# Kernel optimization log

Measured on AMD Instinct MI355X. Metric: run time of the kernel, lower is better.

The kernel has to match this reference:

```python
import jax, jax.numpy as jnp
import numpy as np

LEAKY_SLOPE = 0.2  # tf.nn.leaky_relu default alpha
N_NODES = 50000
N_EDGES = 800000
IN_DIM = 128
OUT_DIM = 64
HEADS = 4
MLP_HID = 256
MLP_OUT = 128


def setup_inputs() -> dict:
    key = jax.random.key(0)
    ks = jax.random.split(key, 10)
    node_embeddings = jax.random.normal(ks[0], (N_NODES, IN_DIM), dtype=jnp.float32)
    src = jax.random.randint(ks[1], (N_EDGES,), 0, N_NODES, dtype=jnp.int32)
    dst = jax.random.randint(ks[2], (N_EDGES,), 0, N_NODES, dtype=jnp.int32)
    # glorot-ish scales
    W_n = jax.random.normal(ks[3], (HEADS, IN_DIM, OUT_DIM), dtype=jnp.float32) * (1.0 / np.sqrt(IN_DIM))
    a_src = jax.random.normal(ks[4], (HEADS, OUT_DIM), dtype=jnp.float32) * (1.0 / np.sqrt(OUT_DIM))
    a_dst = jax.random.normal(ks[5], (HEADS, OUT_DIM), dtype=jnp.float32) * (1.0 / np.sqrt(OUT_DIM))
    mlp_W1 = jax.random.normal(ks[6], (HEADS * OUT_DIM, MLP_HID), dtype=jnp.float32) * (1.0 / np.sqrt(HEADS * OUT_DIM))
    mlp_b1 = jnp.zeros((MLP_HID,), dtype=jnp.float32)
    mlp_W2 = jax.random.normal(ks[7], (MLP_HID, MLP_OUT), dtype=jnp.float32) * (1.0 / np.sqrt(MLP_HID))
    mlp_b2 = jnp.zeros((MLP_OUT,), dtype=jnp.float32)
    return {"node_embeddings": node_embeddings, "src": src, "dst": dst,
            "W_n": W_n, "a_src": a_src, "a_dst": a_dst,
            "mlp_W1": mlp_W1, "mlp_b1": mlp_b1, "mlp_W2": mlp_W2, "mlp_b2": mlp_b2}


def _gat_forward(node_embeddings, src, dst, W_n, a_src, a_dst, mlp_W1, mlp_b1, mlp_W2, mlp_b2):
    N = node_embeddings.shape[0]
    # per-head linear transform: [N, H, D]
    h = jnp.einsum('nc,hcd->nhd', node_embeddings, W_n)
    # decomposed attention scores at node level, gathered per edge
    s_src = jnp.einsum('nhd,hd->nh', h, a_src)          # [N, H]
    s_dst = jnp.einsum('nhd,hd->nh', h, a_dst)          # [N, H]
    e = jax.nn.leaky_relu(s_src[src] + s_dst[dst], negative_slope=LEAKY_SLOPE)  # [E, H]
    # segment softmax over incoming edges of each dst node
    e_max = jax.ops.segment_max(e, dst, num_segments=N)          # [N, H], -inf for empty
    ex = jnp.exp(e - e_max[dst])                                  # [E, H]
    den = jax.ops.segment_sum(ex, dst, num_segments=N)            # [N, H]
    m = h[src]                                                    # [E, H, D] messages
    num = jax.ops.segment_sum(ex[:, :, None] * m, dst, num_segments=N)  # [N, H, D]
    safe_den = jnp.where(den > 0, den, 1.0)
    head_out = jax.nn.relu(num / safe_den[:, :, None])            # [N, H, D]
    concat = head_out.reshape(N, -1)                              # [N, H*D]
    hidden = jax.nn.relu(concat @ mlp_W1 + mlp_b1)
    return hidden @ mlp_W2 + mlp_b2                               # [N, MLP_OUT]


def reference(node_embeddings, src, dst, W_n, a_src, a_dst, mlp_W1, mlp_b1, mlp_W2, mlp_b2):
    return _gat_forward(node_embeddings, src, dst, W_n, a_src, a_dst,
                        mlp_W1, mlp_b1, mlp_W2, mlp_b2)
```

## Files before the change

kernel.cpp:

```cpp
#include <hip/hip_runtime.h>

#define LEAKY 0.2f

typedef __attribute__((ext_vector_type(8))) short short8;
typedef __attribute__((ext_vector_type(4))) float floatx4;

__device__ __forceinline__ float bf2f(unsigned short u) {
    return __uint_as_float(((unsigned)u) << 16);
}
__device__ __forceinline__ unsigned short f2bf(float f) {
    unsigned u = __float_as_uint(f);
    unsigned r = (u + 0x7fffu + ((u >> 16) & 1u)) >> 16;
    return (unsigned short)r;
}
__device__ __forceinline__ float relu_nan(float v) { return v < 0.0f ? 0.0f : v; }

__device__ __forceinline__ void gload_lds16(const void* g, void* l) {
    __builtin_amdgcn_global_load_lds((const __attribute__((address_space(1))) void*)g,
                                     (__attribute__((address_space(3))) void*)l, 16, 0, 0);
}

__global__ void k_fill(float* __restrict__ p, float val, int n) {
    int i = blockIdx.x * blockDim.x + threadIdx.x;
    if (i < n) p[i] = val;
}

__global__ void k_zero(int* __restrict__ cnt, int n) {
    int i = blockIdx.x * blockDim.x + threadIdx.x;
    if (i < n) cnt[i] = 0;
}

__global__ void k_cvt_x(const float* __restrict__ X, unsigned short* __restrict__ Xb, int n4) {
    int i = blockIdx.x * blockDim.x + threadIdx.x;
    if (i < n4) {
        float4 v = ((const float4*)X)[i];
        ushort4 o;
        o.x = f2bf(v.x); o.y = f2bf(v.y); o.z = f2bf(v.z); o.w = f2bf(v.w);
        ((ushort4*)Xb)[i] = o;
    }
}

__global__ void k_cvt_wn(const float* __restrict__ Wn, unsigned short* __restrict__ WnT) {
    int col = blockIdx.x, k = threadIdx.x;
    int head = col >> 6, d = col & 63;
    WnT[(size_t)col * 128 + k] = f2bf(Wn[(size_t)head * 8192 + (size_t)k * 64 + d]);
}

__global__ void k_convert(const float* __restrict__ W, unsigned short* __restrict__ WT, int R, int C) {
    int k = threadIdx.x, n = blockIdx.x;
    WT[(size_t)n * R + k] = f2bf(W[(size_t)k * C + n]);
}

__global__ __launch_bounds__(256) void k_scores(
    const unsigned short* __restrict__ h_bf,
    const float* __restrict__ Asrc, const float* __restrict__ Adst,
    float* __restrict__ s_src, float* __restrict__ s_dst, int N) {
    const int lane = threadIdx.x & 63;
    const int wave = threadIdx.x >> 6;
    const int n = blockIdx.x * 4 + wave;
    if (n >= N) return;
    const int head = lane >> 4;
    const int c0 = lane << 2;
    ushort4 hv = *(const ushort4*)(h_bf + (size_t)n * 256 + c0);
    float4 as = *(const float4*)(Asrc + c0);
    float4 ad = *(const float4*)(Adst + c0);
    float h0 = bf2f(hv.x), h1 = bf2f(hv.y), h2 = bf2f(hv.z), h3 = bf2f(hv.w);
    float ps = h0 * as.x + h1 * as.y + h2 * as.z + h3 * as.w;
    float pd = h0 * ad.x + h1 * ad.y + h2 * ad.z + h3 * ad.w;
    for (int m = 1; m < 16; m <<= 1) {
        ps += __shfl_xor(ps, m, 64);
        pd += __shfl_xor(pd, m, 64);
    }
    if ((lane & 15) == 0) {
        s_src[n * 4 + head] = ps;
        s_dst[n * 4 + head] = pd;
    }
}

__global__ void k_hist(const int* __restrict__ dst, int* __restrict__ cnt, int E) {
    int e = blockIdx.x * blockDim.x + threadIdx.x;
    if (e < E) atomicAdd(cnt + dst[e], 1);
}

__global__ __launch_bounds__(256) void k_scan1(
    const int* __restrict__ cnt, int* __restrict__ rowptr, int* __restrict__ bsum, int N) {
    __shared__ int wtot[4];
    const int lane = threadIdx.x & 63, wave = threadIdx.x >> 6;
    const int i = blockIdx.x * 256 + threadIdx.x;
    int v = (i < N) ? cnt[i] : 0;
    int x = v;
    for (int off = 1; off < 64; off <<= 1) {
        int y = __shfl_up(x, off, 64);
        if (lane >= off) x += y;
    }
    if (lane == 63) wtot[wave] = x;
    __syncthreads();
    int wo = 0;
    for (int wv = 0; wv < wave; ++wv) wo += wtot[wv];
    if (i < N) rowptr[i] = wo + x - v;
    if (threadIdx.x == 255) bsum[blockIdx.x] = wo + x;
}
__global__ void k_scan2(int* __restrict__ bsum, int nb) {
    const int lane = threadIdx.x;
    int carry = 0;
    for (int base = 0; base < nb; base += 64) {
        int i = base + lane;
        int v = (i < nb) ? bsum[i] : 0;
        int x = v;
        for (int off = 1; off < 64; off <<= 1) {
            int y = __shfl_up(x, off, 64);
            if (lane >= off) x += y;
        }
        if (i < nb) bsum[i] = carry + x - v;
        carry += __shfl(x, 63, 64);
    }
}
__global__ void k_scan3(int* __restrict__ rowptr, const int* __restrict__ bsum,
                        int* __restrict__ wcnt, int N, int E) {
    int i = blockIdx.x * blockDim.x + threadIdx.x;
    if (i < N) {
        int v = rowptr[i] + bsum[i >> 8];
        rowptr[i] = v;
        wcnt[i] = v;
    }
    if (i == N) rowptr[N] = E;
}

__global__ void k_scatter(const int* __restrict__ src, const int* __restrict__ dst,
                          int* __restrict__ wcnt, int* __restrict__ esrc, int E) {
    int e = blockIdx.x * blockDim.x + threadIdx.x;
    if (e < E) {
        int pos = atomicAdd(wcnt + dst[e], 1);
        esrc[pos] = src[e];
    }
}

__global__ __launch_bounds__(256) void k_agg(
    const float* __restrict__ s_src, const float* __restrict__ s_dst,
    const unsigned short* __restrict__ h_bf,
    const int* __restrict__ rowptr, const int* __restrict__ esrc,
    unsigned short* __restrict__ concat) {
    const int t = threadIdx.x;
    const int lane = t & 63;
    const int wave = t >> 6;
    const int row0 = blockIdx.x * 16;
    const int head = lane >> 4;
    const int c0 = lane << 2;
    const int eslot = lane & 15;
    const int hsel = lane & 48;

    for (int rr = 0; rr < 4; ++rr) {
        const int n = row0 + wave * 4 + rr;
        const int beg = rowptr[n], end = rowptr[n + 1];
        const float sdst = s_dst[n * 4 + head];
        float num0 = 0, num1 = 0, num2 = 0, num3 = 0, den = 0;
        for (int base = beg; base < end; base += 16) {
            const int nn = end - base;
            int sid = 0;
            float my_ex = 0.0f;
            if (eslot < nn) {
                sid = esrc[base + eslot];
                float v = s_src[sid * 4 + head] + sdst;
                v = v > 0.0f ? v : LEAKY * v;
                my_ex = __expf(v);
            }
#pragma unroll
            for (int e = 0; e < 16; ++e) {
                float ex = __shfl(my_ex, hsel | e, 64);
                int s    = __shfl(sid, e, 64);
                ushort4 hv = *(const ushort4*)(h_bf + (size_t)s * 256 + c0);
                num0 += ex * bf2f(hv.x);
                num1 += ex * bf2f(hv.y);
                num2 += ex * bf2f(hv.z);
                num3 += ex * bf2f(hv.w);
                den  += ex;
            }
        }
        const float inv = 1.0f / (den > 0.0f ? den : 1.0f);
        ushort4 o;
        o.x = f2bf(relu_nan(num0 * inv));
        o.y = f2bf(relu_nan(num1 * inv));
        o.z = f2bf(relu_nan(num2 * inv));
        o.w = f2bf(relu_nan(num3 * inv));
        *(ushort4*)(concat + (size_t)n * 256 + c0) = o;
    }
}

template <int K, int MODE>
__global__ __launch_bounds__(256) void k_gemm(
    const unsigned short* __restrict__ A, const unsigned short* __restrict__ BT,
    const float* __restrict__ bias, unsigned short* __restrict__ Cb,
    float* __restrict__ Cf, int N, int ldout) {
    __shared__ unsigned short As[128 * 32];
    __shared__ unsigned short Bs[128 * 32];
    const int t = threadIdx.x;
    const int lane = t & 63;
    const int w = t >> 6;
    const int wy = w >> 1, wx = w & 1;
    const int lm = lane & 15, quad = lane >> 4;
    const int row0 = blockIdx.x * 128;
    const int n0 = blockIdx.y * 128;
    const int srow = lane >> 2;
    const int sk = (lane & 3) * 8;

    floatx4 acc[4][4];
    if (MODE == 0) {
#pragma unroll
        for (int mi = 0; mi < 4; ++mi)
#pragma unroll
            for (int ni = 0; ni < 4; ++ni) acc[mi][ni] = (floatx4){0, 0, 0, 0};
    } else {
#pragma unroll
        for (int ni = 0; ni < 4; ++ni) {
            float b = bias[n0 + wx * 64 + ni * 16 + lm];
#pragma unroll
            for (int mi = 0; mi < 4; ++mi) acc[mi][ni] = (floatx4){b, b, b, b};
        }
    }

    for (int k0 = 0; k0 < K; k0 += 32) {
#pragma unroll
        for (int p = 0; p < 2; ++p) {
            int tr = (p * 4 + w) * 16 + srow;
            int ga = row0 + tr; if (ga >= N) ga = N - 1;
            gload_lds16(A + (size_t)ga * K + k0 + sk,
                        (char*)As + (size_t)tr * 64 + sk * 2);
            gload_lds16(BT + (size_t)(n0 + tr) * K + k0 + sk,
                        (char*)Bs + (size_t)tr * 64 + sk * 2);
        }
        __syncthreads();
        short8 af[4], bfr[4];
#pragma unroll
        for (int mi = 0; mi < 4; ++mi)
            af[mi] = *(const short8*)(As + (size_t)(wy * 64 + mi * 16 + lm) * 32 + quad * 8);
#pragma unroll
        for (int ni = 0; ni < 4; ++ni)
            bfr[ni] = *(const short8*)(Bs + (size_t)(wx * 64 + ni * 16 + lm) * 32 + quad * 8);
#pragma unroll
        for (int mi = 0; mi < 4; ++mi)
#pragma unroll
            for (int ni = 0; ni < 4; ++ni)
                acc[mi][ni] = __builtin_amdgcn_mfma_f32_16x16x32_bf16(af[mi], bfr[ni], acc[mi][ni], 0, 0, 0);
        __syncthreads();
    }

#pragma unroll
    for (int mi = 0; mi < 4; ++mi)
#pragma unroll
        for (int ni = 0; ni < 4; ++ni)
#pragma unroll
            for (int q = 0; q < 4; ++q) {
                int r = row0 + wy * 64 + mi * 16 + quad * 4 + q;
                int c = n0 + wx * 64 + ni * 16 + lm;
                if (r < N) {
                    if (MODE == 0)      Cb[(size_t)r * ldout + c] = f2bf(acc[mi][ni][q]);
                    else if (MODE == 1) Cb[(size_t)r * ldout + c] = f2bf(relu_nan(acc[mi][ni][q]));
                    else                Cf[(size_t)r * ldout + c] = acc[mi][ni][q];
                }
            }
}

extern "C" void kernel_launch(void* const* d_in, const int* in_sizes, int n_in,
                              void* d_out, int out_size, void* d_ws, size_t ws_size,
                              hipStream_t stream) {
    const float* X    = (const float*)d_in[0];
    const int* src    = (const int*)d_in[1];
    const int* dst    = (const int*)d_in[2];
    const float* Wn   = (const float*)d_in[3];
    const float* Asrc = (const float*)d_in[4];
    const float* Adst = (const float*)d_in[5];
    const float* W1   = (const float*)d_in[6];
    const float* b1   = (const float*)d_in[7];
    const float* W2   = (const float*)d_in[8];
    const float* b2   = (const float*)d_in[9];
    float* out = (float*)d_out;

    const int N = in_sizes[0] / 128;
    const int E = in_sizes[1];
    const int NB = (N + 255) / 256;
    const int NR = (N + 127) / 128;

    size_t off = 0;
    char* w = (char*)d_ws;
    unsigned short* h_bf = (unsigned short*)(w + off); off += (size_t)N * 256 * 2;
    float* s_src = (float*)(w + off);                  off += (size_t)N * 4 * 4;
    float* s_dst = (float*)(w + off);                  off += (size_t)N * 4 * 4;
    int* cnt     = (int*)(w + off);                    off += (size_t)N * 4;
    int* rowptr  = (int*)(w + off);                    off += ((size_t)(N + 1) * 4 + 15) & ~15ull;
    int* wcnt    = (int*)(w + off);                    off += (size_t)N * 4;
    int* bsum    = (int*)(w + off);                    off += ((size_t)NB * 4 + 15) & ~15ull;
    int* esrc    = (int*)(w + off);                    off += (size_t)E * 4;
    unsigned short* W1T = (unsigned short*)(w + off);  off += 256 * 256 * 2;
    unsigned short* W2T = (unsigned short*)(w + off);  off += 128 * 256 * 2;
    unsigned short* WnT = (unsigned short*)(w + off);  off += 256 * 128 * 2;
    const size_t required = off;

    if (ws_size < required) {
        k_fill<<<dim3((out_size + 255) / 256), dim3(256), 0, stream>>>(
            out, (float)(ws_size >> 20), out_size);
        return;
    }

    unsigned short* Xb     = (unsigned short*)d_out;
    unsigned short* concat = (unsigned short*)d_out;

    k_zero<<<dim3((N + 255) / 256), dim3(256), 0, stream>>>(cnt, N);
    k_cvt_x<<<dim3((N * 32 + 255) / 256), dim3(256), 0, stream>>>(X, Xb, N * 32);
    k_cvt_wn<<<dim3(256), dim3(128), 0, stream>>>(Wn, WnT);
    k_gemm<128, 0><<<dim3(NR, 2), dim3(256), 0, stream>>>(Xb, WnT, nullptr, h_bf, nullptr, N, 256);
    k_scores<<<dim3((N + 3) / 4), dim3(256), 0, stream>>>(h_bf, Asrc, Adst, s_src, s_dst, N);
    k_hist<<<dim3((E + 255) / 256), dim3(256), 0, stream>>>(dst, cnt, E);
    k_scan1<<<dim3(NB), dim3(256), 0, stream>>>(cnt, rowptr, bsum, N);
    k_scan2<<<dim3(1), dim3(64), 0, stream>>>(bsum, NB);
    k_scan3<<<dim3((N + 256) / 256), dim3(256), 0, stream>>>(rowptr, bsum, wcnt, N, E);
    k_scatter<<<dim3((E + 255) / 256), dim3(256), 0, stream>>>(src, dst, wcnt, esrc, E);
    k_convert<<<dim3(256), dim3(256), 0, stream>>>(W1, W1T, 256, 256);
    k_convert<<<dim3(128), dim3(256), 0, stream>>>(W2, W2T, 256, 128);
    k_agg<<<dim3(N / 16), dim3(256), 0, stream>>>(s_src, s_dst, h_bf, rowptr, esrc, concat);
    k_gemm<256, 1><<<dim3(NR, 2), dim3(256), 0, stream>>>(concat, W1T, b1, h_bf, nullptr, N, 256);
    k_gemm<256, 2><<<dim3(NR, 1), dim3(256), 0, stream>>>(h_bf, W2T, b2, nullptr, out, N, 128);
}
```

Before: 319.3 us.

## Fuse prep kernels, fold scores into projection GEMM, single-pass decoupled-lookback scan

Merges the zeroing, X conversion and three weight transposes into one grid-stride prep kernel. The attention score computation is moved into the first GEMM's epilogue, using shuffle reductions over the accumulators. The three-kernel scan becomes a single kernel with decoupled lookback through per-block state flags. Together these cut the launch count from 15 to 8 and avoid rereading h for the scores. The trade-off is that the lookback spins on earlier blocks, and the scores now come from fp32 accumulators instead of rounded bf16 values.

```diff
diff --git a/kernel.cpp b/kernel.cpp
--- a/kernel.cpp
+++ b/kernel.cpp
@@ -25,55 +25,34 @@
     if (i < n) p[i] = val;
 }
 
-__global__ void k_zero(int* __restrict__ cnt, int n) {
-    int i = blockIdx.x * blockDim.x + threadIdx.x;
-    if (i < n) cnt[i] = 0;
-}
-
-__global__ void k_cvt_x(const float* __restrict__ X, unsigned short* __restrict__ Xb, int n4) {
-    int i = blockIdx.x * blockDim.x + threadIdx.x;
-    if (i < n4) {
+__global__ void k_prep(const float* __restrict__ X, unsigned short* __restrict__ Xb,
+                       const float* __restrict__ Wn, unsigned short* __restrict__ WnT,
+                       const float* __restrict__ W1, unsigned short* __restrict__ W1T,
+                       const float* __restrict__ W2, unsigned short* __restrict__ W2T,
+                       int* __restrict__ cnt, unsigned long long* __restrict__ state,
+                       int N, int nstate) {
+    const int gs = gridDim.x * blockDim.x;
+    const int tid = blockIdx.x * blockDim.x + threadIdx.x;
+    for (int i = tid; i < N; i += gs) cnt[i] = 0;
+    for (int i = tid; i < nstate; i += gs) state[i] = 0ull;
+    for (int i = tid; i < N * 32; i += gs) {
         float4 v = ((const float4*)X)[i];
         ushort4 o;
         o.x = f2bf(v.x); o.y = f2bf(v.y); o.z = f2bf(v.z); o.w = f2bf(v.w);
         ((ushort4*)Xb)[i] = o;
     }
-}
-
-__global__ void k_cvt_wn(const float* __restrict__ Wn, unsigned short* __restrict__ WnT) {
-    int col = blockIdx.x, k = threadIdx.x;
-    int head = col >> 6, d = col & 63;
-    WnT[(size_t)col * 128 + k] = f2bf(Wn[(size_t)head * 8192 + (size_t)k * 64 + d]);
-}
-
-__global__ void k_convert(const float* __restrict__ W, unsigned short* __restrict__ WT, int R, int C) {
-    int k = threadIdx.x, n = blockIdx.x;
-    WT[(size_t)n * R + k] = f2bf(W[(size_t)k * C + n]);
-}
-
-__global__ __launch_bounds__(256) void k_scores(
-    const unsigned short* __restrict__ h_bf,
-    const float* __restrict__ Asrc, const float* __restrict__ Adst,
-    float* __restrict__ s_src, float* __restrict__ s_dst, int N) {
-    const int lane = threadIdx.x & 63;
-    const int wave = threadIdx.x >> 6;
-    const int n = blockIdx.x * 4 + wave;
-    if (n >= N) return;
-    const int head = lane >> 4;
-    const int c0 = lane << 2;
-    ushort4 hv = *(const ushort4*)(h_bf + (size_t)n * 256 + c0);
-    float4 as = *(const float4*)(Asrc + c0);
-    float4 ad = *(const float4*)(Adst + c0);
-    float h0 = bf2f(hv.x), h1 = bf2f(hv.y), h2 = bf2f(hv.z), h3 = bf2f(hv.w);
-    float ps = h0 * as.x + h1 * as.y + h2 * as.z + h3 * as.w;
-    float pd = h0 * ad.x + h1 * ad.y + h2 * ad.z + h3 * ad.w;
-    for (int m = 1; m < 16; m <<= 1) {
-        ps += __shfl_xor(ps, m, 64);
-        pd += __shfl_xor(pd, m, 64);
-    }
-    if ((lane & 15) == 0) {
-        s_src[n * 4 + head] = ps;
-        s_dst[n * 4 + head] = pd;
+    for (int i = tid; i < 256 * 128; i += gs) {
+        int col = i >> 7, k = i & 127;
+        int head = col >> 6, d = col & 63;
+        WnT[i] = f2bf(Wn[(size_t)head * 8192 + (size_t)k * 64 + d]);
+    }
+    for (int i = tid; i < 256 * 256; i += gs) {
+        int n = i >> 8, k = i & 255;
+        W1T[i] = f2bf(W1[(size_t)k * 256 + n]);
+    }
+    for (int i = tid; i < 128 * 256; i += gs) {
+        int n = i >> 8, k = i & 255;
+        W2T[i] = f2bf(W2[(size_t)k * 128 + n]);
     }
 }
 
@@ -82,11 +61,14 @@
     if (e < E) atomicAdd(cnt + dst[e], 1);
 }
 
-__global__ __launch_bounds__(256) void k_scan1(
-    const int* __restrict__ cnt, int* __restrict__ rowptr, int* __restrict__ bsum, int N) {
+__global__ __launch_bounds__(256) void k_scan_lb(
+    const int* __restrict__ cnt, int* __restrict__ rowptr, int* __restrict__ wcnt,
+    unsigned long long* __restrict__ state, int N, int E, int nblocks) {
     __shared__ int wtot[4];
+    __shared__ int sprefix;
     const int lane = threadIdx.x & 63, wave = threadIdx.x >> 6;
-    const int i = blockIdx.x * 256 + threadIdx.x;
+    const int b = blockIdx.x;
+    const int i = b * 256 + threadIdx.x;
     int v = (i < N) ? cnt[i] : 0;
     int x = v;
     for (int off = 1; off < 64; off <<= 1) {
@@ -97,33 +79,29 @@
     __syncthreads();
     int wo = 0;
     for (int wv = 0; wv < wave; ++wv) wo += wtot[wv];
-    if (i < N) rowptr[i] = wo + x - v;
-    if (threadIdx.x == 255) bsum[blockIdx.x] = wo + x;
-}
-__global__ void k_scan2(int* __restrict__ bsum, int nb) {
-    const int lane = threadIdx.x;
-    int carry = 0;
-    for (int base = 0; base < nb; base += 64) {
-        int i = base + lane;
-        int v = (i < nb) ? bsum[i] : 0;
-        int x = v;
-        for (int off = 1; off < 64; off <<= 1) {
-            int y = __shfl_up(x, off, 64);
-            if (lane >= off) x += y;
-        }
-        if (i < nb) bsum[i] = carry + x - v;
-        carry += __shfl(x, 63, 64);
-    }
-}
-__global__ void k_scan3(int* __restrict__ rowptr, const int* __restrict__ bsum,
-                        int* __restrict__ wcnt, int N, int E) {
-    int i = blockIdx.x * blockDim.x + threadIdx.x;
-    if (i < N) {
-        int v = rowptr[i] + bsum[i >> 8];
-        rowptr[i] = v;
-        wcnt[i] = v;
-    }
-    if (i == N) rowptr[N] = E;
+    const int excl = wo + x - v;
+    if (threadIdx.x == 0) {
+        const int tot = wtot[0] + wtot[1] + wtot[2] + wtot[3];
+        __hip_atomic_store(&state[b], (((unsigned long long)(unsigned)tot) << 2) | 1ull,
+                           __ATOMIC_RELEASE, __HIP_MEMORY_SCOPE_AGENT);
+        unsigned long long run = 0;
+        for (int j = b - 1; j >= 0; --j) {
+            unsigned long long s;
+            do {
+                s = __hip_atomic_load(&state[j], __ATOMIC_ACQUIRE, __HIP_MEMORY_SCOPE_AGENT);
+            } while ((s & 3ull) == 0);
+            run += s >> 2;
+            if (s & 2ull) break;
+        }
+        const int prefix = (int)run;
+        __hip_atomic_store(&state[b], (((unsigned long long)(unsigned)(prefix + tot)) << 2) | 3ull,
+                           __ATOMIC_RELEASE, __HIP_MEMORY_SCOPE_AGENT);
+        sprefix = prefix;
+    }
+    __syncthreads();
+    const int p = sprefix;
+    if (i < N) { rowptr[i] = p + excl; wcnt[i] = p + excl; }
+    if (b == nblocks - 1 && threadIdx.x == 255) rowptr[N] = E;
 }
 
 __global__ void k_scatter(const int* __restrict__ src, const int* __restrict__ dst,
@@ -190,7 +168,9 @@
 __global__ __launch_bounds__(256) void k_gemm(
     const unsigned short* __restrict__ A, const unsigned short* __restrict__ BT,
     const float* __restrict__ bias, unsigned short* __restrict__ Cb,
-    float* __restrict__ Cf, int N, int ldout) {
+    float* __restrict__ Cf, int N, int ldout,
+    const float* __restrict__ asrc, const float* __restrict__ adst,
+    float* __restrict__ s_src, float* __restrict__ s_dst) {
     __shared__ unsigned short As[128 * 32];
     __shared__ unsigned short Bs[128 * 32];
     const int t = threadIdx.x;
@@ -258,6 +238,38 @@
                     else                Cf[(size_t)r * ldout + c] = acc[mi][ni][q];
                 }
             }
+
+    if (MODE == 0) {
+        const int head = blockIdx.y * 2 + wx;
+        float as[4], ad[4];
+#pragma unroll
+        for (int ni = 0; ni < 4; ++ni) {
+            int d = ni * 16 + lm;
+            as[ni] = asrc[head * 64 + d];
+            ad[ni] = adst[head * 64 + d];
+        }
+#pragma unroll
+        for (int mi = 0; mi < 4; ++mi)
+#pragma unroll
+            for (int q = 0; q < 4; ++q) {
+                float ps = acc[mi][0][q] * as[0] + acc[mi][1][q] * as[1]
+                         + acc[mi][2][q] * as[2] + acc[mi][3][q] * as[3];
+                float pd = acc[mi][0][q] * ad[0] + acc[mi][1][q] * ad[1]
+                         + acc[mi][2][q] * ad[2] + acc[mi][3][q] * ad[3];
+#pragma unroll
+                for (int m = 1; m < 16; m <<= 1) {
+                    ps += __shfl_xor(ps, m, 64);
+                    pd += __shfl_xor(pd, m, 64);
+                }
+                if (lm == 0) {
+                    int r = row0 + wy * 64 + mi * 16 + quad * 4 + q;
+                    if (r < N) {
+                        s_src[r * 4 + head] = ps;
+                        s_dst[r * 4 + head] = pd;
+                    }
+                }
+            }
+    }
 }
 
 extern "C" void kernel_launch(void* const* d_in, const int* in_sizes, int n_in,
@@ -277,7 +289,7 @@
 
     const int N = in_sizes[0] / 128;
     const int E = in_sizes[1];
-    const int NB = (N + 255) / 256;
+    const int NBS = (N + 255) / 256;
     const int NR = (N + 127) / 128;
 
     size_t off = 0;
@@ -288,7 +300,7 @@
     int* cnt     = (int*)(w + off);                    off += (size_t)N * 4;
     int* rowptr  = (int*)(w + off);                    off += ((size_t)(N + 1) * 4 + 15) & ~15ull;
     int* wcnt    = (int*)(w + off);                    off += (size_t)N * 4;
-    int* bsum    = (int*)(w + off);                    off += ((size_t)NB * 4 + 15) & ~15ull;
+    unsigned long long* state = (unsigned long long*)(w + off); off += (size_t)NBS * 8;
     int* esrc    = (int*)(w + off);                    off += (size_t)E * 4;
     unsigned short* W1T = (unsigned short*)(w + off);  off += 256 * 256 * 2;
     unsigned short* W2T = (unsigned short*)(w + off);  off += 128 * 256 * 2;
@@ -304,19 +316,16 @@
     unsigned short* Xb     = (unsigned short*)d_out;
     unsigned short* concat = (unsigned short*)d_out;
 
-    k_zero<<<dim3((N + 255) / 256), dim3(256), 0, stream>>>(cnt, N);
-    k_cvt_x<<<dim3((N * 32 + 255) / 256), dim3(256), 0, stream>>>(X, Xb, N * 32);
-    k_cvt_wn<<<dim3(256), dim3(128), 0, stream>>>(Wn, WnT);
-    k_gemm<128, 0><<<dim3(NR, 2), dim3(256), 0, stream>>>(Xb, WnT, nullptr, h_bf, nullptr, N, 256);
-    k_scores<<<dim3((N + 3) / 4), dim3(256), 0, stream>>>(h_bf, Asrc, Adst, s_src, s_dst, N);
+    k_prep<<<dim3(2048), dim3(256), 0, stream>>>(X, Xb, Wn, WnT, W1, W1T, W2, W2T,
+                                                 cnt, state, N, NBS);
+    k_gemm<128, 0><<<dim3(NR, 2), dim3(256), 0, stream>>>(
+        Xb, WnT, nullptr, h_bf, nullptr, N, 256, Asrc, Adst, s_src, s_dst);
     k_hist<<<dim3((E + 255) / 256), dim3(256), 0, stream>>>(dst, cnt, E);
-    k_scan1<<<dim3(NB), dim3(256), 0, stream>>>(cnt, rowptr, bsum, N);
-    k_scan2<<<dim3(1), dim3(64), 0, stream>>>(bsum, NB);
-    k_scan3<<<dim3((N + 256) / 256), dim3(256), 0, stream>>>(rowptr, bsum, wcnt, N, E);
+    k_scan_lb<<<dim3(NBS), dim3(256), 0, stream>>>(cnt, rowptr, wcnt, state, N, E, NBS);
     k_scatter<<<dim3((E + 255) / 256), dim3(256), 0, stream>>>(src, dst, wcnt, esrc, E);
-    k_convert<<<dim3(256), dim3(256), 0, stream>>>(W1, W1T, 256, 256);
-    k_convert<<<dim3(128), dim3(256), 0, stream>>>(W2, W2T, 256, 128);
     k_agg<<<dim3(N / 16), dim3(256), 0, stream>>>(s_src, s_dst, h_bf, rowptr, esrc, concat);
-    k_gemm<256, 1><<<dim3(NR, 2), dim3(256), 0, stream>>>(concat, W1T, b1, h_bf, nullptr, N, 256);
-    k_gemm<256, 2><<<dim3(NR, 1), dim3(256), 0, stream>>>(h_bf, W2T, b2, nullptr, out, N, 128);
-}
+    k_gemm<256, 1><<<dim3(NR, 2), dim3(256), 0, stream>>>(
+        concat, W1T, b1, h_bf, nullptr, N, 256, nullptr, nullptr, nullptr, nullptr);
+    k_gemm<256, 2><<<dim3(NR, 1), dim3(256), 0, stream>>>(
+        h_bf, W2T, b2, nullptr, out, N, 128, nullptr, nullptr, nullptr, nullptr);
+}
```

Result: slower. 337.9 us (+5.8%).
